# Kernel optimization log

Measured on AMD Instinct MI355X. Metric: run time of the kernel, lower is better.

Reference implementation:

```python
import jax, jax.numpy as jnp
import numpy as np

B, D, N, E = 4, 128, 16384, 65536  # batch, feature_dim, n_junctions, 2*n_lines
EPS = 1e-5  # BatchNorm eps


def setup_inputs() -> dict:
    key = jax.random.key(0)
    ks = jax.random.split(key, 8)
    s = lambda k, shape: jax.random.normal(k, shape, dtype=jnp.float32)
    return {
        "ldesc0": s(ks[0], (B, D, N)),
        "ldesc1": s(ks[1], (B, D, N)),
        "line_enc0": s(ks[2], (B, D, E)),
        "line_enc1": s(ks[3], (B, D, E)),
        "lines_junc_idx0": jax.random.randint(ks[4], (B, E), 0, N),
        "lines_junc_idx1": jax.random.randint(ks[5], (B, E), 0, N),
        # MLP([3D, 2D, D]) params: conv1x1 -> BN -> ReLU -> conv1x1
        "w1": s(ks[6], (2 * D, 3 * D)) * 0.05,
        "b1": jnp.zeros((2 * D,), jnp.float32),
        "bn_gamma": jnp.ones((2 * D,), jnp.float32),
        "bn_beta": jnp.zeros((2 * D,), jnp.float32),
        "bn_mean": jnp.zeros((2 * D,), jnp.float32),
        "bn_var": jnp.ones((2 * D,), jnp.float32),
        "w2": s(ks[7], (D, 2 * D)) * 0.05,
        "b2": jnp.zeros((D,), jnp.float32),
    }


def _mlp(x, w1, b1, g, beta, mu, var, w2, b2):
    # x: [B, 3D, E] -> [B, D, E]; BN in inference mode with running stats
    h = jnp.einsum('oi,bie->boe', w1, x) + b1[None, :, None]
    scale = g / jnp.sqrt(var + EPS)
    h = h * scale[None, :, None] + (beta - mu * scale)[None, :, None]
    h = jax.nn.relu(h)
    return jnp.einsum('oi,bie->boe', w2, h) + b2[None, :, None]


def _endpoint_update(ldesc, line_enc, idx, params):
    # gather endpoint descriptors: [B, D, E]
    line_desc = jax.vmap(lambda x, i: x[:, i])(ldesc, idx)
    b, d, e = line_desc.shape
    # swap the two endpoints of each line (flip along the size-2 axis)
    flipped = line_desc.reshape(b, d, e // 2, 2)[..., ::-1].reshape(b, d, e)
    message = jnp.concatenate([line_desc, flipped, line_enc], axis=1)  # [B, 3D, E]
    return _mlp(message, *params)


def _scatter_mean(src, idx, n):
    # src: [B, D, E], idx: [B, E] -> mean-reduced [B, D, n]; empty slots stay 0
    def one(s, i):
        sums = jax.ops.segment_sum(s.T, i, num_segments=n)                    # [n, D]
        cnt = jax.ops.segment_sum(jnp.ones(s.shape[1], s.dtype), i, num_segments=n)
        return (sums / jnp.maximum(cnt, 1.0)[:, None]).T                      # [D, n]
    return jax.vmap(one)(src, idx)


def reference(ldesc0, ldesc1, line_enc0, line_enc1, lines_junc_idx0, lines_junc_idx1,
              w1, b1, bn_gamma, bn_beta, bn_mean, bn_var, w2, b2):
    params = (w1, b1, bn_gamma, bn_beta, bn_mean, bn_var, w2, b2)
    up0 = _endpoint_update(ldesc0, line_enc0, lines_junc_idx0, params)
    up1 = _endpoint_update(ldesc1, line_enc1, lines_junc_idx1, params)
    n = ldesc0.shape[2]
    out0 = ldesc0 + _scatter_mean(up0, lines_junc_idx0, n)
    out1 = ldesc1 + _scatter_mean(up1, lines_junc_idx1, n)
    return (out0, out1)
```

## Files before the change

kernel.cpp:

```cpp
#include <hip/hip_runtime.h>
#include <hip/hip_bf16.h>
#include <stdint.h>

#define Bb 4
#define Dd 128
#define Nn 16384
#define Ee 65536
#define NTB 16

typedef __attribute__((ext_vector_type(4))) float f32x4;
typedef __attribute__((ext_vector_type(8))) short s16x8;

__device__ __forceinline__ unsigned short f2bf(float f) {
  union { float f; unsigned int u; } v; v.f = f;
  unsigned int r = v.u + 0x7fffu + ((v.u >> 16) & 1u);
  return (unsigned short)(r >> 16);
}

__global__ void prep_weights(const float* __restrict__ w1, const float* __restrict__ b1,
                             const float* __restrict__ g, const float* __restrict__ beta,
                             const float* __restrict__ mu, const float* __restrict__ var,
                             const float* __restrict__ w2,
                             unsigned short* __restrict__ W1s, unsigned short* __restrict__ W2s,
                             float* __restrict__ c1) {
  int i = blockIdx.x * 256 + threadIdx.x;
  if (i < 256 * 384) {
    int o = i / 384;
    float scale = g[o] * rsqrtf(var[o] + 1e-5f);
    W1s[i] = f2bf(w1[i] * scale);
  }
  if (i < 128 * 256) W2s[i] = f2bf(w2[i]);
  if (i < 256) {
    float scale = g[i] * rsqrtf(var[i] + 1e-5f);
    c1[i] = b1[i] * scale + beta[i] - mu[i] * scale;
  }
}

__global__ void transpose_f2b(const float* __restrict__ src, unsigned short* __restrict__ dst,
                              int ncols) {
  __shared__ float tile[32][33];
  int n0 = blockIdx.x * 32;
  int d0 = blockIdx.y * 32;
  int b = blockIdx.z;
  const float* s = src + (size_t)b * Dd * ncols;
  unsigned short* d = dst + (size_t)b * ncols * Dd;
  int tx = threadIdx.x, ty = threadIdx.y;
#pragma unroll
  for (int i = 0; i < 4; ++i)
    tile[ty + i * 8][tx] = s[(size_t)(d0 + ty + i * 8) * ncols + n0 + tx];
  __syncthreads();
#pragma unroll
  for (int i = 0; i < 4; ++i) {
    int r = ty + i * 8;
    d[(size_t)(n0 + r) * Dd + d0 + tx] = f2bf(tile[tx][r]);
  }
}

__global__ void hist_kernel(const int* __restrict__ idx0, const int* __restrict__ idx1,
                            int* __restrict__ hist) {
  int i = blockIdx.x * 256 + threadIdx.x;
  int sb = i >> 16;
  int e = i & 65535;
  const int* jx = (sb >= 4) ? idx1 : idx0;
  int n = jx[(size_t)(sb & 3) * Ee + e];
  atomicAdd(&hist[sb * Nn + n], 1);
}

__global__ __launch_bounds__(1024) void scan_kernel(const int* __restrict__ hist,
                                                    int* __restrict__ offs,
                                                    int* __restrict__ cursor) {
  __shared__ int part[1024];
  int sb = blockIdx.x, t = threadIdx.x;
  const int* h = hist + sb * Nn;
  int base = t * 16;
  int v[16];
  int local = 0;
#pragma unroll
  for (int i = 0; i < 16; ++i) { v[i] = local; local += h[base + i]; }
  part[t] = local;
  __syncthreads();
  for (int d = 1; d < 1024; d <<= 1) {
    int y = (t >= d) ? part[t - d] : 0;
    __syncthreads();
    part[t] += y;
    __syncthreads();
  }
  int excl = part[t] - local;
#pragma unroll
  for (int i = 0; i < 16; ++i) {
    int o = excl + v[i];
    offs[sb * Nn + base + i] = o;
    cursor[sb * Nn + base + i] = o;
  }
}

__global__ void fill_kernel(const int* __restrict__ idx0, const int* __restrict__ idx1,
                            int* __restrict__ cursor, int* __restrict__ elist) {
  int i = blockIdx.x * 256 + threadIdx.x;
  int sb = i >> 16;
  int e = i & 65535;
  const int* jx = (sb >= 4) ? idx1 : idx0;
  int n = jx[(size_t)(sb & 3) * Ee + e];
  int pos = atomicAdd(&cursor[sb * Nn + n], 1);
  elist[(size_t)sb * Ee + pos] = e;
}

#define STAGE(ti, buf)                                                          \
  do {                                                                          \
    int e0s_ = (tile0 + (ti)) * 64;                                             \
    unsigned char* xb_ = sm + (buf) * 32768;                                    \
    int cA_ = w * 8 + (lane >> 4);                                              \
    int cB_ = cA_ + 4;                                                          \
    int uA_ = (lane & 15) ^ (cA_ & 7);                                          \
    int uB_ = (lane & 15) ^ (cB_ & 7);                                          \
    int iA_ = jx[(size_t)bB * Ee + e0s_ + cA_];                                 \
    int iB_ = jx[(size_t)bB * Ee + e0s_ + cB_];                                 \
    __builtin_amdgcn_global_load_lds(                                           \
        (const __attribute__((address_space(1))) void*)(ldescT + ((size_t)bB * Nn + iA_) * 128 + uA_ * 8), \
        (__attribute__((address_space(3))) void*)(xb_ + (w * 8) * 256), 16, 0, 0); \
    __builtin_amdgcn_global_load_lds(                                           \
        (const __attribute__((address_space(1))) void*)(ldescT + ((size_t)bB * Nn + iB_) * 128 + uB_ * 8), \
        (__attribute__((address_space(3))) void*)(xb_ + (w * 8 + 4) * 256), 16, 0, 0); \
    __builtin_amdgcn_global_load_lds(                                           \
        (const __attribute__((address_space(1))) void*)(encT + ((size_t)bB * Ee + e0s_ + cA_) * 128 + uA_ * 8), \
        (__attribute__((address_space(3))) void*)(xb_ + 16384 + (w * 8) * 256), 16, 0, 0); \
    __builtin_amdgcn_global_load_lds(                                           \
        (const __attribute__((address_space(1))) void*)(encT + ((size_t)bB * Ee + e0s_ + cB_) * 128 + uB_ * 8), \
        (__attribute__((address_space(3))) void*)(xb_ + 16384 + (w * 8 + 4) * 256), 16, 0, 0); \
  } while (0)

__global__ __launch_bounds__(512, 2) void fused_mlp_ws(
    const unsigned short* __restrict__ ldescT,
    const unsigned short* __restrict__ encT,
    const int* __restrict__ jx,
    const unsigned short* __restrict__ W1s, const unsigned short* __restrict__ W2s,
    const float* __restrict__ c1, const float* __restrict__ b2,
    unsigned short* __restrict__ U) {
  __shared__ __align__(16) unsigned char sm[98304];

  const int t = threadIdx.x;
  const int w = t >> 6;
  const int lane = t & 63;
  const int lr = t & 15;
  const int lk = (t & 63) >> 4;
  const int bB = blockIdx.x >> 6;
  const int tile0 = (blockIdx.x & 63) * NTB;

  s16x8 w1f[2][12];
#pragma unroll
  for (int rt = 0; rt < 2; ++rt)
#pragma unroll
    for (int ks = 0; ks < 12; ++ks)
      w1f[rt][ks] = *(const s16x8*)&W1s[(size_t)(w * 32 + rt * 16 + lr) * 384 + ks * 32 + lk * 8];
  s16x8 w2f[8];
#pragma unroll
  for (int ks = 0; ks < 8; ++ks)
    w2f[ks] = *(const s16x8*)&W2s[(size_t)(w * 16 + lr) * 256 + ks * 32 + lk * 8];
  float c1v[2][4], b2v[4];
#pragma unroll
  for (int rt = 0; rt < 2; ++rt)
#pragma unroll
    for (int r = 0; r < 4; ++r) c1v[rt][r] = c1[w * 32 + rt * 16 + lk * 4 + r];
#pragma unroll
  for (int r = 0; r < 4; ++r) b2v[r] = b2[w * 16 + lk * 4 + r];

  STAGE(0, 0);
  STAGE(1, 1);
  asm volatile("s_waitcnt vmcnt(4)" ::: "memory");
  __builtin_amdgcn_s_barrier();
  __builtin_amdgcn_sched_barrier(0);

  unsigned short* hb = (unsigned short*)(sm + 65536);

#pragma unroll 1
  for (int i = 0; i < NTB; ++i) {
    const int p = i & 1;
    const unsigned short* xb = (const unsigned short*)(sm + p * 32768);
    const int e0c = (tile0 + i) * 64;

    f32x4 acc[2][4] = {};
#pragma unroll
    for (int ks = 0; ks < 12; ++ks) {
      s16x8 bf[4];
#pragma unroll
      for (int ct = 0; ct < 4; ++ct) {
        int c = ct * 16 + lr;
        int off;
        if (ks < 4)      { off = c * 128 + (((ks * 4 + lk) ^ (c & 7)) * 8); }
        else if (ks < 8) { int c2 = c ^ 1; off = c2 * 128 + ((((ks - 4) * 4 + lk) ^ (c2 & 7)) * 8); }
        else             { off = 8192 + c * 128 + ((((ks - 8) * 4 + lk) ^ (c & 7)) * 8); }
        bf[ct] = *(const s16x8*)&xb[off];
      }
#pragma unroll
      for (int rt = 0; rt < 2; ++rt)
#pragma unroll
        for (int ct = 0; ct < 4; ++ct)
          acc[rt][ct] = __builtin_amdgcn_mfma_f32_16x16x32_bf16(w1f[rt][ks], bf[ct], acc[rt][ct], 0, 0, 0);
    }

#pragma unroll
    for (int rt = 0; rt < 2; ++rt) {
      int rowbase = w * 32 + rt * 16 + lk * 4;
      int unitr = rowbase >> 3, inner = rowbase & 7;
#pragma unroll
      for (int ct = 0; ct < 4; ++ct) {
        int col = ct * 16 + lr;
        float v0 = fmaxf(acc[rt][ct][0] + c1v[rt][0], 0.f);
        float v1 = fmaxf(acc[rt][ct][1] + c1v[rt][1], 0.f);
        float v2 = fmaxf(acc[rt][ct][2] + c1v[rt][2], 0.f);
        float v3 = fmaxf(acc[rt][ct][3] + c1v[rt][3], 0.f);
        uint2 pk;
        pk.x = (unsigned int)f2bf(v0) | ((unsigned int)f2bf(v1) << 16);
        pk.y = (unsigned int)f2bf(v2) | ((unsigned int)f2bf(v3) << 16);
        *(uint2*)&hb[col * 256 + ((unitr ^ (col & 7)) * 8) + inner] = pk;
      }
    }
    asm volatile("s_waitcnt lgkmcnt(0)" ::: "memory");
    __builtin_amdgcn_s_barrier();
    __builtin_amdgcn_sched_barrier(0);

    if (i + 2 < NTB) STAGE(i + 2, p);

    f32x4 acc2[4] = {};
#pragma unroll
    for (int ks = 0; ks < 8; ++ks) {
      s16x8 bf[4];
#pragma unroll
      for (int ct = 0; ct < 4; ++ct) {
        int c = ct * 16 + lr;
        bf[ct] = *(const s16x8*)&hb[c * 256 + (((ks * 4 + lk) ^ (c & 7)) * 8)];
      }
#pragma unroll
      for (int ct = 0; ct < 4; ++ct)
        acc2[ct] = __builtin_amdgcn_mfma_f32_16x16x32_bf16(w2f[ks], bf[ct], acc2[ct], 0, 0, 0);
    }

#pragma unroll
    for (int ct = 0; ct < 4; ++ct) {
      int col = ct * 16 + lr;
      float v0 = acc2[ct][0] + b2v[0];
      float v1 = acc2[ct][1] + b2v[1];
      float v2 = acc2[ct][2] + b2v[2];
      float v3 = acc2[ct][3] + b2v[3];
      uint2 pk;
      pk.x = (unsigned int)f2bf(v0) | ((unsigned int)f2bf(v1) << 16);
      pk.y = (unsigned int)f2bf(v2) | ((unsigned int)f2bf(v3) << 16);
      *(uint2*)&U[(((size_t)bB * Ee + e0c + col) << 7) + w * 16 + lk * 4] = pk;
    }

    if (i + 1 < NTB) {
      asm volatile("s_waitcnt lgkmcnt(0)" ::: "memory");
      asm volatile("s_waitcnt vmcnt(8)" ::: "memory");
      __builtin_amdgcn_s_barrier();
      __builtin_amdgcn_sched_barrier(0);
    }
  }
}

__device__ __forceinline__ int swz(int col, int unit) { return col * 32 + (unit ^ (col & 7)); }

__global__ __launch_bounds__(256, 4) void fused_line_mlp_fb(
    const unsigned short* __restrict__ ldescT, const float* __restrict__ enc,
    const int* __restrict__ jx,
    const unsigned short* __restrict__ W1s, const unsigned short* __restrict__ W2s,
    const float* __restrict__ c1, const float* __restrict__ b2,
    unsigned short* __restrict__ U) {
  __shared__ uint4 smem4[64 * 32];
  unsigned short* sm = (unsigned short*)smem4;
  const int b = blockIdx.y;
  const int e0 = blockIdx.x * 64;
  const int t = threadIdx.x;
  {
    int j = t >> 2, p = t & 3;
    int i0 = jx[(size_t)b * Ee + e0 + j];
    const uint4* s0 = (const uint4*)(ldescT + ((size_t)b * Nn + i0) * Dd + p * 32);
#pragma unroll
    for (int q = 0; q < 4; ++q) smem4[swz(j, p * 4 + q)] = s0[q];
  }
  {
    int j = t & 63, dg = t >> 6;
    const float* src = enc + ((size_t)b * Dd + dg * 32) * Ee + e0 + j;
#pragma unroll
    for (int i8 = 0; i8 < 4; ++i8) {
      uint4 pk;
      unsigned int* pw = (unsigned int*)&pk;
#pragma unroll
      for (int d2 = 0; d2 < 4; ++d2) {
        float f0 = src[(size_t)(i8 * 8 + d2 * 2) * Ee];
        float f1 = src[(size_t)(i8 * 8 + d2 * 2 + 1) * Ee];
        pw[d2] = (unsigned int)f2bf(f0) | ((unsigned int)f2bf(f1) << 16);
      }
      smem4[swz(j, 16 + dg * 4 + i8)] = pk;
    }
  }
  __syncthreads();
  const int w = t >> 6, lr = t & 15, lk = (t & 63) >> 4;
  f32x4 acc[4][4] = {};
#pragma unroll
  for (int ks = 0; ks < 12; ++ks) {
    s16x8 bfrag[4];
#pragma unroll
    for (int ct = 0; ct < 4; ++ct) {
      int c = ct * 16 + lr;
      int ce, bu;
      if (ks < 4)      { ce = c;     bu = ks * 4 + lk; }
      else if (ks < 8) { ce = c ^ 1; bu = (ks - 4) * 4 + lk; }
      else             { ce = c;     bu = 16 + (ks - 8) * 4 + lk; }
      bfrag[ct] = *(const s16x8*)&sm[swz(ce, bu) * 8];
    }
#pragma unroll
    for (int rt = 0; rt < 4; ++rt) {
      const s16x8 afrag = *(const s16x8*)&W1s[(size_t)(w * 64 + rt * 16 + lr) * 384 + ks * 32 + lk * 8];
#pragma unroll
      for (int ct = 0; ct < 4; ++ct)
        acc[rt][ct] = __builtin_amdgcn_mfma_f32_16x16x32_bf16(afrag, bfrag[ct], acc[rt][ct], 0, 0, 0);
    }
  }
  __syncthreads();
#pragma unroll
  for (int rt = 0; rt < 4; ++rt) {
    int rowbase = w * 64 + rt * 16 + lk * 4;
    int unit = rowbase >> 3, inner = rowbase & 7;
    float c1v[4];
#pragma unroll
    for (int r = 0; r < 4; ++r) c1v[r] = c1[rowbase + r];
#pragma unroll
    for (int ct = 0; ct < 4; ++ct) {
      int col = ct * 16 + lr;
      float v0 = fmaxf(acc[rt][ct][0] + c1v[0], 0.f);
      float v1 = fmaxf(acc[rt][ct][1] + c1v[1], 0.f);
      float v2 = fmaxf(acc[rt][ct][2] + c1v[2], 0.f);
      float v3 = fmaxf(acc[rt][ct][3] + c1v[3], 0.f);
      uint2 pk;
      pk.x = (unsigned int)f2bf(v0) | ((unsigned int)f2bf(v1) << 16);
      pk.y = (unsigned int)f2bf(v2) | ((unsigned int)f2bf(v3) << 16);
      *(uint2*)&sm[swz(col, unit) * 8 + inner] = pk;
    }
  }
  __syncthreads();
  f32x4 acc2[2][4] = {};
#pragma unroll
  for (int ks = 0; ks < 8; ++ks) {
    s16x8 bfrag[4];
#pragma unroll
    for (int ct = 0; ct < 4; ++ct) {
      int c = ct * 16 + lr;
      bfrag[ct] = *(const s16x8*)&sm[swz(c, ks * 4 + lk) * 8];
    }
#pragma unroll
    for (int rt = 0; rt < 2; ++rt) {
      const s16x8 afrag = *(const s16x8*)&W2s[(size_t)(w * 32 + rt * 16 + lr) * 256 + ks * 32 + lk * 8];
#pragma unroll
      for (int ct = 0; ct < 4; ++ct)
        acc2[rt][ct] = __builtin_amdgcn_mfma_f32_16x16x32_bf16(afrag, bfrag[ct], acc2[rt][ct], 0, 0, 0);
    }
  }
#pragma unroll
  for (int rt = 0; rt < 2; ++rt) {
    int rowbase = w * 32 + rt * 16 + lk * 4;
    float b2v[4];
#pragma unroll
    for (int r = 0; r < 4; ++r) b2v[r] = b2[rowbase + r];
#pragma unroll
    for (int ct = 0; ct < 4; ++ct) {
      int col = ct * 16 + lr;
      float v0 = acc2[rt][ct][0] + b2v[0];
      float v1 = acc2[rt][ct][1] + b2v[1];
      float v2 = acc2[rt][ct][2] + b2v[2];
      float v3 = acc2[rt][ct][3] + b2v[3];
      uint2 pk;
      pk.x = (unsigned int)f2bf(v0) | ((unsigned int)f2bf(v1) << 16);
      pk.y = (unsigned int)f2bf(v2) | ((unsigned int)f2bf(v3) << 16);
      *(uint2*)&U[(((size_t)b * Ee + e0 + col) << 7) + rowbase] = pk;
    }
  }
}

__global__ __launch_bounds__(256) void scatter_finalize(
    const unsigned short* __restrict__ U, const int* __restrict__ elist_s,
    const int* __restrict__ offs_s, const float* __restrict__ ldesc_s,
    float* __restrict__ out_s) {
  __shared__ float lsum[64][129];
  const int b = blockIdx.y;
  const int n0 = blockIdx.x * 64;
  const int t = threadIdx.x;
  const int w = t >> 6, lane = t & 63;
  const unsigned int* Uu = (const unsigned int*)U;

#pragma unroll 1
  for (int q = 0; q < 16; ++q) {
    int jj = w * 16 + q;
    int n = n0 + jj;
    int s = offs_s[b * Nn + n];
    int e_end = (n == Nn - 1) ? Ee : offs_s[b * Nn + n + 1];
    float s0 = 0.f, s1 = 0.f;
    for (int k = s; k < e_end; ++k) {
      int e = elist_s[(size_t)b * Ee + k];
      unsigned int p = Uu[(((size_t)b * Ee + e) << 6) + lane];
      union { unsigned int u; float f; } lo, hi;
      lo.u = p << 16;
      hi.u = p & 0xffff0000u;
      s0 += lo.f;
      s1 += hi.f;
    }
    float inv = (e_end > s) ? 1.0f / (float)(e_end - s) : 0.0f;
    lsum[jj][lane * 2] = s0 * inv;
    lsum[jj][lane * 2 + 1] = s1 * inv;
  }
  __syncthreads();

  int nloc = t & 63;
  int dbase = (t >> 6) * 32;
#pragma unroll
  for (int i = 0; i < 32; ++i) {
    int d = dbase + i;
    size_t o = (size_t)(b * Dd + d) * Nn + n0 + nloc;
    out_s[o] = ldesc_s[o] + lsum[nloc][d];
  }
}

extern "C" void kernel_launch(void* const* d_in, const int* in_sizes, int n_in,
                              void* d_out, int out_size, void* d_ws, size_t ws_size,
                              hipStream_t stream) {
  const float* ldesc0 = (const float*)d_in[0];
  const float* ldesc1 = (const float*)d_in[1];
  const float* enc0   = (const float*)d_in[2];
  const float* enc1   = (const float*)d_in[3];
  const int*   idx0   = (const int*)d_in[4];
  const int*   idx1   = (const int*)d_in[5];
  const float* w1     = (const float*)d_in[6];
  const float* b1     = (const float*)d_in[7];
  const float* g      = (const float*)d_in[8];
  const float* beta   = (const float*)d_in[9];
  const float* mu     = (const float*)d_in[10];
  const float* var    = (const float*)d_in[11];
  const float* w2     = (const float*)d_in[12];
  const float* b2     = (const float*)d_in[13];
  float* out = (float*)d_out;

  char* ws = (char*)d_ws;
  size_t off = 0;
  unsigned short* t   = (unsigned short*)(ws + off); off += (size_t)Bb * Nn * Dd * 2;
  unsigned short* W1s = (unsigned short*)(ws + off); off += 256 * 384 * 2;
  unsigned short* W2s = (unsigned short*)(ws + off); off += 128 * 256 * 2;
  float* c1   = (float*)(ws + off); off += 256 * 4;
  int* hist   = (int*)(ws + off); off += (size_t)8 * Nn * 4;
  int* offs   = (int*)(ws + off); off += (size_t)8 * Nn * 4;
  int* cursor = (int*)(ws + off); off += (size_t)8 * Nn * 4;
  int* elist  = (int*)(ws + off); off += (size_t)8 * Ee * 4;
  unsigned short* U = (unsigned short*)(ws + off); off += (size_t)Bb * Ee * Dd * 2;
  unsigned short* encT = (unsigned short*)(ws + off);
  size_t need_new = off + (size_t)Bb * Ee * Dd * 2;

  hipMemsetAsync(hist, 0, (size_t)8 * Nn * 4, stream);
  prep_weights<<<384, 256, 0, stream>>>(w1, b1, g, beta, mu, var, w2, W1s, W2s, c1);
  hist_kernel<<<2048, 256, 0, stream>>>(idx0, idx1, hist);
  scan_kernel<<<8, 1024, 0, stream>>>(hist, offs, cursor);
  fill_kernel<<<2048, 256, 0, stream>>>(idx0, idx1, cursor, elist);

  const bool use_new = (ws_size >= need_new);

  for (int side = 0; side < 2; ++side) {
    const float* ldesc_s = side ? ldesc1 : ldesc0;
    const float* enc_s = side ? enc1 : enc0;
    const int* jx = side ? idx1 : idx0;
    transpose_f2b<<<dim3(Nn / 32, Dd / 32, Bb), dim3(32, 8), 0, stream>>>(ldesc_s, t, Nn);
    if (use_new) {
      transpose_f2b<<<dim3(Ee / 32, Dd / 32, Bb), dim3(32, 8), 0, stream>>>(enc_s, encT, Ee);
      fused_mlp_ws<<<256, 512, 0, stream>>>(t, encT, jx, W1s, W2s, c1, b2, U);
    } else {
      fused_line_mlp_fb<<<dim3(Ee / 64, Bb), 256, 0, stream>>>(t, enc_s, jx, W1s, W2s, c1, b2, U);
    }
    scatter_finalize<<<dim3(Nn / 64, Bb), 256, 0, stream>>>(
        U, elist + (size_t)side * 4 * Ee, offs + (size_t)side * 4 * Nn,
        ldesc_s, out + (size_t)side * Bb * Dd * Nn);
  }
}
```

Measured before the change: 451.0 us.

## Batch both sides into single launches and add packed bf16 conversion

Merges the per-side transpose, fused MLP and scatter launches into single launches that cover both sides, so each grid doubles in size and the device is filled better. This needs double-size workspace buffers, and the per-side loop is kept as a fallback when the workspace is too small. It also switches bf16 packing to the hardware v_cvt_pk_bf16_f32 instruction, raises wave priority around the MFMA loops, and writes the MLP output U with nontemporal stores. The old fallback MLP kernel is removed and the per-side path now uses the staged kernel.

```diff
diff --git a/kernel.cpp b/kernel.cpp
--- a/kernel.cpp
+++ b/kernel.cpp
@@ -10,11 +10,18 @@
 
 typedef __attribute__((ext_vector_type(4))) float f32x4;
 typedef __attribute__((ext_vector_type(8))) short s16x8;
+typedef __attribute__((ext_vector_type(2))) unsigned int u32x2;
 
 __device__ __forceinline__ unsigned short f2bf(float f) {
   union { float f; unsigned int u; } v; v.f = f;
   unsigned int r = v.u + 0x7fffu + ((v.u >> 16) & 1u);
   return (unsigned short)(r >> 16);
+}
+
+__device__ __forceinline__ unsigned int cvtpk(float lo, float hi) {
+  unsigned int r;
+  asm volatile("v_cvt_pk_bf16_f32 %0, %1, %2" : "=v"(r) : "v"(lo), "v"(hi));
+  return r;
 }
 
 __global__ void prep_weights(const float* __restrict__ w1, const float* __restrict__ b1,
@@ -36,23 +43,34 @@
   }
 }
 
-__global__ void transpose_f2b(const float* __restrict__ src, unsigned short* __restrict__ dst,
-                              int ncols) {
+__global__ void transpose_all(const float* __restrict__ l0, const float* __restrict__ l1,
+                              const float* __restrict__ e0, const float* __restrict__ e1,
+                              unsigned short* __restrict__ t, unsigned short* __restrict__ encT) {
   __shared__ float tile[32][33];
-  int n0 = blockIdx.x * 32;
+  int zb = blockIdx.z, side = zb >> 2, b = zb & 3;
+  int bx = blockIdx.x;
+  const float* src;
+  unsigned short* dst;
+  int ncols, n0;
+  if (bx < Nn / 32) {
+    src = (side ? l1 : l0) + (size_t)b * Dd * Nn;
+    dst = t + ((size_t)(side * Bb + b)) * Nn * Dd;
+    ncols = Nn; n0 = bx * 32;
+  } else {
+    src = (side ? e1 : e0) + (size_t)b * Dd * Ee;
+    dst = encT + ((size_t)(side * Bb + b)) * Ee * Dd;
+    ncols = Ee; n0 = (bx - Nn / 32) * 32;
+  }
   int d0 = blockIdx.y * 32;
-  int b = blockIdx.z;
-  const float* s = src + (size_t)b * Dd * ncols;
-  unsigned short* d = dst + (size_t)b * ncols * Dd;
   int tx = threadIdx.x, ty = threadIdx.y;
 #pragma unroll
   for (int i = 0; i < 4; ++i)
-    tile[ty + i * 8][tx] = s[(size_t)(d0 + ty + i * 8) * ncols + n0 + tx];
+    tile[ty + i * 8][tx] = src[(size_t)(d0 + ty + i * 8) * ncols + n0 + tx];
   __syncthreads();
 #pragma unroll
   for (int i = 0; i < 4; ++i) {
     int r = ty + i * 8;
-    d[(size_t)(n0 + r) * Dd + d0 + tx] = f2bf(tile[tx][r]);
+    dst[(size_t)(n0 + r) * Dd + d0 + tx] = f2bf(tile[tx][r]);
   }
 }
 
@@ -113,26 +131,26 @@
     int cB_ = cA_ + 4;                                                          \
     int uA_ = (lane & 15) ^ (cA_ & 7);                                          \
     int uB_ = (lane & 15) ^ (cB_ & 7);                                          \
-    int iA_ = jx[(size_t)bB * Ee + e0s_ + cA_];                                 \
-    int iB_ = jx[(size_t)bB * Ee + e0s_ + cB_];                                 \
+    int iA_ = jxB[e0s_ + cA_];                                                  \
+    int iB_ = jxB[e0s_ + cB_];                                                  \
     __builtin_amdgcn_global_load_lds(                                           \
-        (const __attribute__((address_space(1))) void*)(ldescT + ((size_t)bB * Nn + iA_) * 128 + uA_ * 8), \
+        (const __attribute__((address_space(1))) void*)(ldB + ((size_t)iA_) * 128 + uA_ * 8), \
         (__attribute__((address_space(3))) void*)(xb_ + (w * 8) * 256), 16, 0, 0); \
     __builtin_amdgcn_global_load_lds(                                           \
-        (const __attribute__((address_space(1))) void*)(ldescT + ((size_t)bB * Nn + iB_) * 128 + uB_ * 8), \
+        (const __attribute__((address_space(1))) void*)(ldB + ((size_t)iB_) * 128 + uB_ * 8), \
         (__attribute__((address_space(3))) void*)(xb_ + (w * 8 + 4) * 256), 16, 0, 0); \
     __builtin_amdgcn_global_load_lds(                                           \
-        (const __attribute__((address_space(1))) void*)(encT + ((size_t)bB * Ee + e0s_ + cA_) * 128 + uA_ * 8), \
+        (const __attribute__((address_space(1))) void*)(enB + ((size_t)(e0s_ + cA_)) * 128 + uA_ * 8), \
         (__attribute__((address_space(3))) void*)(xb_ + 16384 + (w * 8) * 256), 16, 0, 0); \
     __builtin_amdgcn_global_load_lds(                                           \
-        (const __attribute__((address_space(1))) void*)(encT + ((size_t)bB * Ee + e0s_ + cB_) * 128 + uB_ * 8), \
+        (const __attribute__((address_space(1))) void*)(enB + ((size_t)(e0s_ + cB_)) * 128 + uB_ * 8), \
         (__attribute__((address_space(3))) void*)(xb_ + 16384 + (w * 8 + 4) * 256), 16, 0, 0); \
   } while (0)
 
 __global__ __launch_bounds__(512, 2) void fused_mlp_ws(
     const unsigned short* __restrict__ ldescT,
     const unsigned short* __restrict__ encT,
-    const int* __restrict__ jx,
+    const int* __restrict__ idx0, const int* __restrict__ idx1, int side0,
     const unsigned short* __restrict__ W1s, const unsigned short* __restrict__ W2s,
     const float* __restrict__ c1, const float* __restrict__ b2,
     unsigned short* __restrict__ U) {
@@ -143,8 +161,15 @@
   const int lane = t & 63;
   const int lr = t & 15;
   const int lk = (t & 63) >> 4;
-  const int bB = blockIdx.x >> 6;
+  const int ls = blockIdx.x >> 8;
+  const int gs = side0 + ls;
+  const int bB = (blockIdx.x >> 6) & 3;
   const int tile0 = (blockIdx.x & 63) * NTB;
+
+  const int* jxB = (gs ? idx1 : idx0) + (size_t)bB * Ee;
+  const unsigned short* ldB = ldescT + ((size_t)(ls * Bb + bB)) * Nn * 128;
+  const unsigned short* enB = encT + ((size_t)(ls * Bb + bB)) * Ee * 128;
+  unsigned short* UB = U + ((size_t)(ls * Bb + bB)) * Ee * 128;
 
   s16x8 w1f[2][12];
 #pragma unroll
@@ -179,6 +204,7 @@
     const int e0c = (tile0 + i) * 64;
 
     f32x4 acc[2][4] = {};
+    __builtin_amdgcn_s_setprio(1);
 #pragma unroll
     for (int ks = 0; ks < 12; ++ks) {
       s16x8 bf[4];
@@ -197,6 +223,7 @@
         for (int ct = 0; ct < 4; ++ct)
           acc[rt][ct] = __builtin_amdgcn_mfma_f32_16x16x32_bf16(w1f[rt][ks], bf[ct], acc[rt][ct], 0, 0, 0);
     }
+    __builtin_amdgcn_s_setprio(0);
 
 #pragma unroll
     for (int rt = 0; rt < 2; ++rt) {
@@ -210,8 +237,8 @@
         float v2 = fmaxf(acc[rt][ct][2] + c1v[rt][2], 0.f);
         float v3 = fmaxf(acc[rt][ct][3] + c1v[rt][3], 0.f);
         uint2 pk;
-        pk.x = (unsigned int)f2bf(v0) | ((unsigned int)f2bf(v1) << 16);
-        pk.y = (unsigned int)f2bf(v2) | ((unsigned int)f2bf(v3) << 16);
+        pk.x = cvtpk(v0, v1);
+        pk.y = cvtpk(v2, v3);
         *(uint2*)&hb[col * 256 + ((unitr ^ (col & 7)) * 8) + inner] = pk;
       }
     }
@@ -222,6 +249,7 @@
     if (i + 2 < NTB) STAGE(i + 2, p);
 
     f32x4 acc2[4] = {};
+    __builtin_amdgcn_s_setprio(1);
 #pragma unroll
     for (int ks = 0; ks < 8; ++ks) {
       s16x8 bf[4];
@@ -234,18 +262,15 @@
       for (int ct = 0; ct < 4; ++ct)
         acc2[ct] = __builtin_amdgcn_mfma_f32_16x16x32_bf16(w2f[ks], bf[ct], acc2[ct], 0, 0, 0);
     }
+    __builtin_amdgcn_s_setprio(0);
 
 #pragma unroll
     for (int ct = 0; ct < 4; ++ct) {
       int col = ct * 16 + lr;
-      float v0 = acc2[ct][0] + b2v[0];
-      float v1 = acc2[ct][1] + b2v[1];
-      float v2 = acc2[ct][2] + b2v[2];
-      float v3 = acc2[ct][3] + b2v[3];
-      uint2 pk;
-      pk.x = (unsigned int)f2bf(v0) | ((unsigned int)f2bf(v1) << 16);
-      pk.y = (unsigned int)f2bf(v2) | ((unsigned int)f2bf(v3) << 16);
-      *(uint2*)&U[(((size_t)bB * Ee + e0c + col) << 7) + w * 16 + lk * 4] = pk;
+      u32x2 pk;
+      pk[0] = cvtpk(acc2[ct][0] + b2v[0], acc2[ct][1] + b2v[1]);
+      pk[1] = cvtpk(acc2[ct][2] + b2v[2], acc2[ct][3] + b2v[3]);
+      __builtin_nontemporal_store(pk, (u32x2*)&UB[(((size_t)(e0c + col)) << 7) + w * 16 + lk * 4]);
     }
 
     if (i + 1 < NTB) {
@@ -257,146 +282,33 @@
   }
 }
 
-__device__ __forceinline__ int swz(int col, int unit) { return col * 32 + (unit ^ (col & 7)); }
-
-__global__ __launch_bounds__(256, 4) void fused_line_mlp_fb(
-    const unsigned short* __restrict__ ldescT, const float* __restrict__ enc,
-    const int* __restrict__ jx,
-    const unsigned short* __restrict__ W1s, const unsigned short* __restrict__ W2s,
-    const float* __restrict__ c1, const float* __restrict__ b2,
-    unsigned short* __restrict__ U) {
-  __shared__ uint4 smem4[64 * 32];
-  unsigned short* sm = (unsigned short*)smem4;
-  const int b = blockIdx.y;
-  const int e0 = blockIdx.x * 64;
-  const int t = threadIdx.x;
-  {
-    int j = t >> 2, p = t & 3;
-    int i0 = jx[(size_t)b * Ee + e0 + j];
-    const uint4* s0 = (const uint4*)(ldescT + ((size_t)b * Nn + i0) * Dd + p * 32);
-#pragma unroll
-    for (int q = 0; q < 4; ++q) smem4[swz(j, p * 4 + q)] = s0[q];
-  }
-  {
-    int j = t & 63, dg = t >> 6;
-    const float* src = enc + ((size_t)b * Dd + dg * 32) * Ee + e0 + j;
-#pragma unroll
-    for (int i8 = 0; i8 < 4; ++i8) {
-      uint4 pk;
-      unsigned int* pw = (unsigned int*)&pk;
-#pragma unroll
-      for (int d2 = 0; d2 < 4; ++d2) {
-        float f0 = src[(size_t)(i8 * 8 + d2 * 2) * Ee];
-        float f1 = src[(size_t)(i8 * 8 + d2 * 2 + 1) * Ee];
-        pw[d2] = (unsigned int)f2bf(f0) | ((unsigned int)f2bf(f1) << 16);
-      }
-      smem4[swz(j, 16 + dg * 4 + i8)] = pk;
-    }
-  }
-  __syncthreads();
-  const int w = t >> 6, lr = t & 15, lk = (t & 63) >> 4;
-  f32x4 acc[4][4] = {};
-#pragma unroll
-  for (int ks = 0; ks < 12; ++ks) {
-    s16x8 bfrag[4];
-#pragma unroll
-    for (int ct = 0; ct < 4; ++ct) {
-      int c = ct * 16 + lr;
-      int ce, bu;
-      if (ks < 4)      { ce = c;     bu = ks * 4 + lk; }
-      else if (ks < 8) { ce = c ^ 1; bu = (ks - 4) * 4 + lk; }
-      else             { ce = c;     bu = 16 + (ks - 8) * 4 + lk; }
-      bfrag[ct] = *(const s16x8*)&sm[swz(ce, bu) * 8];
-    }
-#pragma unroll
-    for (int rt = 0; rt < 4; ++rt) {
-      const s16x8 afrag = *(const s16x8*)&W1s[(size_t)(w * 64 + rt * 16 + lr) * 384 + ks * 32 + lk * 8];
-#pragma unroll
-      for (int ct = 0; ct < 4; ++ct)
-        acc[rt][ct] = __builtin_amdgcn_mfma_f32_16x16x32_bf16(afrag, bfrag[ct], acc[rt][ct], 0, 0, 0);
-    }
-  }
-  __syncthreads();
-#pragma unroll
-  for (int rt = 0; rt < 4; ++rt) {
-    int rowbase = w * 64 + rt * 16 + lk * 4;
-    int unit = rowbase >> 3, inner = rowbase & 7;
-    float c1v[4];
-#pragma unroll
-    for (int r = 0; r < 4; ++r) c1v[r] = c1[rowbase + r];
-#pragma unroll
-    for (int ct = 0; ct < 4; ++ct) {
-      int col = ct * 16 + lr;
-      float v0 = fmaxf(acc[rt][ct][0] + c1v[0], 0.f);
-      float v1 = fmaxf(acc[rt][ct][1] + c1v[1], 0.f);
-      float v2 = fmaxf(acc[rt][ct][2] + c1v[2], 0.f);
-      float v3 = fmaxf(acc[rt][ct][3] + c1v[3], 0.f);
-      uint2 pk;
-      pk.x = (unsigned int)f2bf(v0) | ((unsigned int)f2bf(v1) << 16);
-      pk.y = (unsigned int)f2bf(v2) | ((unsigned int)f2bf(v3) << 16);
-      *(uint2*)&sm[swz(col, unit) * 8 + inner] = pk;
-    }
-  }
-  __syncthreads();
-  f32x4 acc2[2][4] = {};
-#pragma unroll
-  for (int ks = 0; ks < 8; ++ks) {
-    s16x8 bfrag[4];
-#pragma unroll
-    for (int ct = 0; ct < 4; ++ct) {
-      int c = ct * 16 + lr;
-      bfrag[ct] = *(const s16x8*)&sm[swz(c, ks * 4 + lk) * 8];
-    }
-#pragma unroll
-    for (int rt = 0; rt < 2; ++rt) {
-      const s16x8 afrag = *(const s16x8*)&W2s[(size_t)(w * 32 + rt * 16 + lr) * 256 + ks * 32 + lk * 8];
-#pragma unroll
-      for (int ct = 0; ct < 4; ++ct)
-        acc2[rt][ct] = __builtin_amdgcn_mfma_f32_16x16x32_bf16(afrag, bfrag[ct], acc2[rt][ct], 0, 0, 0);
-    }
-  }
-#pragma unroll
-  for (int rt = 0; rt < 2; ++rt) {
-    int rowbase = w * 32 + rt * 16 + lk * 4;
-    float b2v[4];
-#pragma unroll
-    for (int r = 0; r < 4; ++r) b2v[r] = b2[rowbase + r];
-#pragma unroll
-    for (int ct = 0; ct < 4; ++ct) {
-      int col = ct * 16 + lr;
-      float v0 = acc2[rt][ct][0] + b2v[0];
-      float v1 = acc2[rt][ct][1] + b2v[1];
-      float v2 = acc2[rt][ct][2] + b2v[2];
-      float v3 = acc2[rt][ct][3] + b2v[3];
-      uint2 pk;
-      pk.x = (unsigned int)f2bf(v0) | ((unsigned int)f2bf(v1) << 16);
-      pk.y = (unsigned int)f2bf(v2) | ((unsigned int)f2bf(v3) << 16);
-      *(uint2*)&U[(((size_t)b * Ee + e0 + col) << 7) + rowbase] = pk;
-    }
-  }
-}
-
 __global__ __launch_bounds__(256) void scatter_finalize(
-    const unsigned short* __restrict__ U, const int* __restrict__ elist_s,
-    const int* __restrict__ offs_s, const float* __restrict__ ldesc_s,
-    float* __restrict__ out_s) {
+    const unsigned short* __restrict__ U, const int* __restrict__ elist,
+    const int* __restrict__ offs, const float* __restrict__ l0,
+    const float* __restrict__ l1, float* __restrict__ out, int side0) {
   __shared__ float lsum[64][129];
+  const int ls = blockIdx.z;
+  const int gs = side0 + ls;
   const int b = blockIdx.y;
   const int n0 = blockIdx.x * 64;
   const int t = threadIdx.x;
   const int w = t >> 6, lane = t & 63;
-  const unsigned int* Uu = (const unsigned int*)U;
+  const unsigned int* Uu = (const unsigned int*)(U + ((size_t)(ls * Bb + b)) * Ee * 128);
+  const int* elist_s = elist + ((size_t)(gs * Bb + b)) * Ee;
+  const int* offs_s = offs + ((size_t)(gs * Bb + b)) * Nn;
+  const float* l = (gs ? l1 : l0) + (size_t)b * Dd * Nn;
+  float* o = out + ((size_t)(gs * Bb + b)) * Dd * Nn;
 
 #pragma unroll 1
   for (int q = 0; q < 16; ++q) {
     int jj = w * 16 + q;
     int n = n0 + jj;
-    int s = offs_s[b * Nn + n];
-    int e_end = (n == Nn - 1) ? Ee : offs_s[b * Nn + n + 1];
+    int s = offs_s[n];
+    int e_end = (n == Nn - 1) ? Ee : offs_s[n + 1];
     float s0 = 0.f, s1 = 0.f;
     for (int k = s; k < e_end; ++k) {
-      int e = elist_s[(size_t)b * Ee + k];
-      unsigned int p = Uu[(((size_t)b * Ee + e) << 6) + lane];
+      int e = elist_s[k];
+      unsigned int p = Uu[(((size_t)e) << 6) + lane];
       union { unsigned int u; float f; } lo, hi;
       lo.u = p << 16;
       hi.u = p & 0xffff0000u;
@@ -414,8 +326,8 @@
 #pragma unroll
   for (int i = 0; i < 32; ++i) {
     int d = dbase + i;
-    size_t o = (size_t)(b * Dd + d) * Nn + n0 + nloc;
-    out_s[o] = ldesc_s[o] + lsum[nloc][d];
+    size_t off2 = (size_t)d * Nn + n0 + nloc;
+    o[off2] = l[off2] + lsum[nloc][d];
   }
 }
 
@@ -440,7 +352,6 @@
 
   char* ws = (char*)d_ws;
   size_t off = 0;
-  unsigned short* t   = (unsigned short*)(ws + off); off += (size_t)Bb * Nn * Dd * 2;
   unsigned short* W1s = (unsigned short*)(ws + off); off += 256 * 384 * 2;
   unsigned short* W2s = (unsigned short*)(ws + off); off += 128 * 256 * 2;
   float* c1   = (float*)(ws + off); off += 256 * 4;
@@ -448,9 +359,17 @@
   int* offs   = (int*)(ws + off); off += (size_t)8 * Nn * 4;
   int* cursor = (int*)(ws + off); off += (size_t)8 * Nn * 4;
   int* elist  = (int*)(ws + off); off += (size_t)8 * Ee * 4;
-  unsigned short* U = (unsigned short*)(ws + off); off += (size_t)Bb * Ee * Dd * 2;
-  unsigned short* encT = (unsigned short*)(ws + off);
-  size_t need_new = off + (size_t)Bb * Ee * Dd * 2;
+  size_t small_end = off;
+
+  const size_t tside = (size_t)Bb * Nn * Dd * 2;
+  const size_t bigside = (size_t)Bb * Ee * Dd * 2;
+  size_t need_full = small_end + 2 * tside + 4 * bigside;
+  const bool full = (ws_size >= need_full);
+  const int sides_buf = full ? 2 : 1;
+
+  unsigned short* t    = (unsigned short*)(ws + off); off += tside * sides_buf;
+  unsigned short* U    = (unsigned short*)(ws + off); off += bigside * sides_buf;
+  unsigned short* encT = (unsigned short*)(ws + off); off += bigside * sides_buf;
 
   hipMemsetAsync(hist, 0, (size_t)8 * Nn * 4, stream);
   prep_weights<<<384, 256, 0, stream>>>(w1, b1, g, beta, mu, var, w2, W1s, W2s, c1);
@@ -458,21 +377,21 @@
   scan_kernel<<<8, 1024, 0, stream>>>(hist, offs, cursor);
   fill_kernel<<<2048, 256, 0, stream>>>(idx0, idx1, cursor, elist);
 
-  const bool use_new = (ws_size >= need_new);
-
-  for (int side = 0; side < 2; ++side) {
-    const float* ldesc_s = side ? ldesc1 : ldesc0;
-    const float* enc_s = side ? enc1 : enc0;
-    const int* jx = side ? idx1 : idx0;
-    transpose_f2b<<<dim3(Nn / 32, Dd / 32, Bb), dim3(32, 8), 0, stream>>>(ldesc_s, t, Nn);
-    if (use_new) {
-      transpose_f2b<<<dim3(Ee / 32, Dd / 32, Bb), dim3(32, 8), 0, stream>>>(enc_s, encT, Ee);
-      fused_mlp_ws<<<256, 512, 0, stream>>>(t, encT, jx, W1s, W2s, c1, b2, U);
-    } else {
-      fused_line_mlp_fb<<<dim3(Ee / 64, Bb), 256, 0, stream>>>(t, enc_s, jx, W1s, W2s, c1, b2, U);
-    }
-    scatter_finalize<<<dim3(Nn / 64, Bb), 256, 0, stream>>>(
-        U, elist + (size_t)side * 4 * Ee, offs + (size_t)side * 4 * Nn,
-        ldesc_s, out + (size_t)side * Bb * Dd * Nn);
-  }
-}
+  if (full) {
+    transpose_all<<<dim3(Nn / 32 + Ee / 32, Dd / 32, 8), dim3(32, 8), 0, stream>>>(
+        ldesc0, ldesc1, enc0, enc1, t, encT);
+    fused_mlp_ws<<<512, 512, 0, stream>>>(t, encT, idx0, idx1, 0, W1s, W2s, c1, b2, U);
+    scatter_finalize<<<dim3(Nn / 64, Bb, 2), 256, 0, stream>>>(
+        U, elist, offs, ldesc0, ldesc1, out, 0);
+  } else {
+    for (int side = 0; side < 2; ++side) {
+      const float* ldesc_s = side ? ldesc1 : ldesc0;
+      const float* enc_s = side ? enc1 : enc0;
+      transpose_all<<<dim3(Nn / 32 + Ee / 32, Dd / 32, 4), dim3(32, 8), 0, stream>>>(
+          ldesc_s, ldesc_s, enc_s, enc_s, t, encT);
+      fused_mlp_ws<<<256, 512, 0, stream>>>(t, encT, idx0, idx1, side, W1s, W2s, c1, b2, U);
+      scatter_finalize<<<dim3(Nn / 64, Bb, 1), 256, 0, stream>>>(
+          U, elist, offs, ldesc0, ldesc1, out, side);
+    }
+  }
+}
```

New measurement: 502.9 us. +11.5%, slower.
